# Optimization experiments

Hardware: AMD Instinct MI355X
Metric: run time of the kernel (lower is better)

The kernel has to match this reference:

```python
import jax, jax.numpy as jnp
import numpy as np

N_NODES = 50000
N_EDGES = 800000
DIM = 128
N_LAYERS = 5


def setup_inputs() -> dict:
    key = jax.random.key(0)
    k1, k2, k3, k4 = jax.random.split(key, 4)
    x = jax.random.normal(k1, (N_NODES, DIM), dtype=jnp.float32)
    edge_index = jax.random.randint(k2, (2, N_EDGES), 0, N_NODES, dtype=jnp.int64)
    # He-ish scale for stacked GCN layers so activations stay sane
    weights = jax.random.normal(k3, (N_LAYERS, DIM, DIM), dtype=jnp.float32) / jnp.sqrt(jnp.float32(DIM))
    biases = jax.random.normal(k4, (N_LAYERS, DIM), dtype=jnp.float32) * 0.01
    return {"x": x, "edge_index": edge_index, "weights": weights, "biases": biases}


def reference(x, edge_index, weights, biases):
    """5x (GCNConv -> ReLU). GCNConv: out = D^-1/2 (A+I) D^-1/2 (x W) + b."""
    n = x.shape[0]
    src, dst = edge_index[0], edge_index[1]
    # add self-loops (PyG GCNConv default)
    loop = jnp.arange(n, dtype=src.dtype)
    src_f = jnp.concatenate([src, loop])
    dst_f = jnp.concatenate([dst, loop])
    # symmetric normalization based on in-degree (incl. self loops)
    deg = jax.ops.segment_sum(jnp.ones(src_f.shape[0], dtype=x.dtype), dst_f, num_segments=n)
    dinv = jnp.where(deg > 0, jax.lax.rsqrt(deg), 0.0)
    norm = dinv[src_f] * dinv[dst_f]  # [E+N]

    for l in range(weights.shape[0]):
        h = x @ weights[l]                      # [N, D] dense transform
        msg = h[src_f] * norm[:, None]          # gather + scale  [E+N, D]
        x = jax.ops.segment_sum(msg, dst_f, num_segments=n) + biases[l]
        x = jax.nn.relu(x)
    return x
```

## Files before the change

kernel.cpp:

```cpp
#include <hip/hip_runtime.h>
#include <hip/hip_bf16.h>
#include <hip/hip_fp16.h>


#define GCN_DIM 128

typedef short bf16x8 __attribute__((ext_vector_type(8)));
typedef float f32x4 __attribute__((ext_vector_type(4)));

__device__ __forceinline__ unsigned short f2bf(float f) {
    unsigned int u = __float_as_uint(f);
    u += 0x7FFFu + ((u >> 16) & 1u);
    return (unsigned short)(u >> 16);
}
__device__ __forceinline__ float bf2f(unsigned short b) {
    return __uint_as_float(((unsigned int)b) << 16);
}
__device__ __forceinline__ float bflo(unsigned int p) { return __uint_as_float(p << 16); }
__device__ __forceinline__ float bfhi(unsigned int p) { return __uint_as_float(p & 0xFFFF0000u); }

__global__ void init_kernel(int* __restrict__ cnt, int n) {
    int i = blockIdx.x * 256 + threadIdx.x;
    if (i < n) cnt[i] = 0;
}

__global__ void count_kernel(const int* __restrict__ dst, int* __restrict__ cnt,
                             int* __restrict__ rank, int E) {
    int e = blockIdx.x * 256 + threadIdx.x;
    if (e < E) rank[e] = atomicAdd(&cnt[dst[e]], 1);
}

__global__ __launch_bounds__(256) void scan_part_kernel(const int* __restrict__ cnt,
                                                        int* __restrict__ loc,
                                                        int* __restrict__ bsum, int n) {
    __shared__ int s[256];
    int t = threadIdx.x;
    int i0 = blockIdx.x * 1024 + t * 4;
    int v0 = (i0 + 0 < n) ? cnt[i0 + 0] : 0;
    int v1 = (i0 + 1 < n) ? cnt[i0 + 1] : 0;
    int v2 = (i0 + 2 < n) ? cnt[i0 + 2] : 0;
    int v3 = (i0 + 3 < n) ? cnt[i0 + 3] : 0;
    int tsum = v0 + v1 + v2 + v3;
    s[t] = tsum;
    __syncthreads();
    for (int d = 1; d < 256; d <<= 1) {
        int u = (t >= d) ? s[t - d] : 0;
        __syncthreads();
        s[t] += u;
        __syncthreads();
    }
    int base = s[t] - tsum;
    if (i0 + 0 < n) loc[i0 + 0] = base; base += v0;
    if (i0 + 1 < n) loc[i0 + 1] = base; base += v1;
    if (i0 + 2 < n) loc[i0 + 2] = base; base += v2;
    if (i0 + 3 < n) loc[i0 + 3] = base;
    if (t == 255) bsum[blockIdx.x] = s[255];
}

__global__ __launch_bounds__(256) void scan_top_kernel(int* __restrict__ bsum, int nb) {
    __shared__ int s[256];
    int t = threadIdx.x;
    int v = (t < nb) ? bsum[t] : 0;
    s[t] = v;
    __syncthreads();
    for (int d = 1; d < 256; d <<= 1) {
        int u = (t >= d) ? s[t - d] : 0;
        __syncthreads();
        s[t] += u;
        __syncthreads();
    }
    if (t < nb) bsum[t] = s[t] - v;
}

__global__ void scan_add_kernel(int* __restrict__ offs,
                                const int* __restrict__ bsum, const int* __restrict__ cnt,
                                float* __restrict__ dinv, int n, int E) {
    int i = blockIdx.x * 256 + threadIdx.x;
    if (i < n) {
        offs[i] = offs[i] + bsum[i >> 10];
        dinv[i] = rsqrtf((float)cnt[i] + 1.0f);
    }
    if (i == 0) offs[n] = E;
}

__global__ void fill_kernel(const int* __restrict__ src, const int* __restrict__ dst,
                            const float* __restrict__ dinv, const int* __restrict__ rank,
                            const int* __restrict__ offs,
                            unsigned int* __restrict__ edat, int E) {
    int e = blockIdx.x * 256 + threadIdx.x;
    if (e < E) {
        int d = dst[e];
        int s = src[e];
        int p = offs[d] + rank[e];
        unsigned short wb = __half_as_ushort(__float2half(dinv[s]));
        edat[p] = (unsigned int)s | ((unsigned int)wb << 16);
    }
}

__global__ void split_x_kernel(const float* __restrict__ x, unsigned short* __restrict__ xh,
                               unsigned short* __restrict__ xl, int total) {
    int i = (blockIdx.x * 256 + threadIdx.x) * 4;
    if (i >= total) return;
    float4 v = *(const float4*)&x[i];
    ushort4 h4, l4;
    h4.x = f2bf(v.x); l4.x = f2bf(v.x - bf2f(h4.x));
    h4.y = f2bf(v.y); l4.y = f2bf(v.y - bf2f(h4.y));
    h4.z = f2bf(v.z); l4.z = f2bf(v.z - bf2f(h4.z));
    h4.w = f2bf(v.w); l4.w = f2bf(v.w - bf2f(h4.w));
    *(ushort4*)&xh[i] = h4;
    *(ushort4*)&xl[i] = l4;
}

__global__ void wsplit_kernel(const float* __restrict__ Wall, unsigned short* __restrict__ Wfh,
                              unsigned short* __restrict__ Wfl, int total) {
    int idx = blockIdx.x * 256 + threadIdx.x;
    if (idx >= total) return;
    int l = idx >> 14;
    int rem = idx & 16383;
    int k = rem >> 7;
    int nn = rem & 127;
    float v = Wall[idx];
    unsigned short hi = f2bf(v);
    unsigned short lo = f2bf(v - bf2f(hi));
    int t = nn >> 4, ln = nn & 15;
    int ks = k >> 5, q = (k >> 3) & 3, j = k & 7;
    int o = ((((l << 5) | (t << 2) | ks) << 6) | (q << 4) | ln) * 8 + j;
    Wfh[o] = hi;
    Wfl[o] = lo;
}

__global__ __launch_bounds__(256) void gemm_mfma_kernel(
    const unsigned short* __restrict__ xh, const unsigned short* __restrict__ xl,
    const unsigned short* __restrict__ Wfh, const unsigned short* __restrict__ Wfl,
    unsigned short* __restrict__ h, int n) {
    __shared__ unsigned short ldsW[2][8192];
    int tid = threadIdx.x;
    int wave = tid >> 6, lane = tid & 63;
    int q = lane >> 4, ln = lane & 15;
    int rowbase = blockIdx.x * 128 + wave * 32;
    bf16x8 A[2][4][2];
#pragma unroll
    for (int m = 0; m < 2; m++) {
        int ar = rowbase + m * 16 + ln;
        if (ar >= n) ar = n - 1;
        size_t base = (size_t)ar * GCN_DIM;
#pragma unroll
        for (int ks = 0; ks < 4; ks++) {
            A[m][ks][0] = *(const bf16x8*)&xh[base + ks * 32 + q * 8];
            A[m][ks][1] = *(const bf16x8*)&xl[base + ks * 32 + q * 8];
        }
    }
#pragma unroll
    for (int half = 0; half < 2; half++) {
        if (half) __syncthreads();
        {
            const uint4* gh = (const uint4*)(Wfh + half * 8192);
            const uint4* gl = (const uint4*)(Wfl + half * 8192);
            uint4* sh = (uint4*)ldsW[0];
            uint4* sl = (uint4*)ldsW[1];
#pragma unroll
            for (int r = 0; r < 4; r++) {
                sh[tid + 256 * r] = gh[tid + 256 * r];
                sl[tid + 256 * r] = gl[tid + 256 * r];
            }
        }
        __syncthreads();
#pragma unroll
        for (int tt = 0; tt < 4; tt++) {
            int t = half * 4 + tt;
            f32x4 acc0 = (f32x4)(0.f), acc1 = (f32x4)(0.f);
#pragma unroll
            for (int ks = 0; ks < 4; ks++) {
                int fo = ((tt * 4 + ks) * 64 + lane) * 8;
                bf16x8 bh = *(const bf16x8*)&ldsW[0][fo];
                bf16x8 bl = *(const bf16x8*)&ldsW[1][fo];
                acc0 = __builtin_amdgcn_mfma_f32_16x16x32_bf16(A[0][ks][0], bh, acc0, 0, 0, 0);
                acc1 = __builtin_amdgcn_mfma_f32_16x16x32_bf16(A[1][ks][0], bh, acc1, 0, 0, 0);
                acc0 = __builtin_amdgcn_mfma_f32_16x16x32_bf16(A[0][ks][1], bh, acc0, 0, 0, 0);
                acc1 = __builtin_amdgcn_mfma_f32_16x16x32_bf16(A[1][ks][1], bh, acc1, 0, 0, 0);
                acc0 = __builtin_amdgcn_mfma_f32_16x16x32_bf16(A[0][ks][0], bl, acc0, 0, 0, 0);
                acc1 = __builtin_amdgcn_mfma_f32_16x16x32_bf16(A[1][ks][0], bl, acc1, 0, 0, 0);
            }
#pragma unroll
            for (int m = 0; m < 2; m++) {
                f32x4 a = m ? acc1 : acc0;
#pragma unroll
                for (int r = 0; r < 4; r++) {
                    int row = rowbase + m * 16 + q * 4 + r;
                    if (row < n) h[(size_t)row * GCN_DIM + t * 16 + ln] = f2bf(a[r]);
                }
            }
        }
    }
}

__global__ __launch_bounds__(256) void agg_kernel(
    const unsigned short* __restrict__ h,
    const unsigned int* __restrict__ edat,
    const int* __restrict__ offs,
    const float* __restrict__ dinv, const float* __restrict__ bias,
    unsigned short* __restrict__ xh_out,
    unsigned short* __restrict__ xl_out,
    float* __restrict__ fout, int n) {
    int tid = threadIdx.x;
    int wave = tid >> 6, lane = tid & 63;
    int sub = lane >> 4, ln = lane & 15;
    int slice = blockIdx.x & 3;
    int node = (blockIdx.x >> 2) * 16 + wave * 4 + sub;
    if (node >= n) return;
    int co = slice * 32 + ln * 2;
    float di = dinv[node];
    unsigned int sp = *(const unsigned int*)&h[((size_t)node << 7) + co];
    float ax0 = di * bflo(sp), ay0 = di * bfhi(sp);
    float ax1 = 0.f, ay1 = 0.f, ax2 = 0.f, ay2 = 0.f, ax3 = 0.f, ay3 = 0.f;
    int s = offs[node], e = offs[node + 1];
    int j = s;
    for (; j + 8 <= e; j += 8) {
        unsigned int v0 = edat[j], v1 = edat[j + 1], v2 = edat[j + 2], v3 = edat[j + 3];
        unsigned int v4 = edat[j + 4], v5 = edat[j + 5], v6 = edat[j + 6], v7 = edat[j + 7];
        unsigned int p0 = *(const unsigned int*)&h[((size_t)(v0 & 0xFFFFu) << 7) + co];
        unsigned int p1 = *(const unsigned int*)&h[((size_t)(v1 & 0xFFFFu) << 7) + co];
        unsigned int p2 = *(const unsigned int*)&h[((size_t)(v2 & 0xFFFFu) << 7) + co];
        unsigned int p3 = *(const unsigned int*)&h[((size_t)(v3 & 0xFFFFu) << 7) + co];
        unsigned int p4 = *(const unsigned int*)&h[((size_t)(v4 & 0xFFFFu) << 7) + co];
        unsigned int p5 = *(const unsigned int*)&h[((size_t)(v5 & 0xFFFFu) << 7) + co];
        unsigned int p6 = *(const unsigned int*)&h[((size_t)(v6 & 0xFFFFu) << 7) + co];
        unsigned int p7 = *(const unsigned int*)&h[((size_t)(v7 & 0xFFFFu) << 7) + co];
        float w0 = __half2float(__ushort_as_half((unsigned short)(v0 >> 16)));
        float w1 = __half2float(__ushort_as_half((unsigned short)(v1 >> 16)));
        float w2 = __half2float(__ushort_as_half((unsigned short)(v2 >> 16)));
        float w3 = __half2float(__ushort_as_half((unsigned short)(v3 >> 16)));
        float w4 = __half2float(__ushort_as_half((unsigned short)(v4 >> 16)));
        float w5 = __half2float(__ushort_as_half((unsigned short)(v5 >> 16)));
        float w6 = __half2float(__ushort_as_half((unsigned short)(v6 >> 16)));
        float w7 = __half2float(__ushort_as_half((unsigned short)(v7 >> 16)));
        ax0 = fmaf(w0, bflo(p0), ax0); ay0 = fmaf(w0, bfhi(p0), ay0);
        ax1 = fmaf(w1, bflo(p1), ax1); ay1 = fmaf(w1, bfhi(p1), ay1);
        ax2 = fmaf(w2, bflo(p2), ax2); ay2 = fmaf(w2, bfhi(p2), ay2);
        ax3 = fmaf(w3, bflo(p3), ax3); ay3 = fmaf(w3, bfhi(p3), ay3);
        ax0 = fmaf(w4, bflo(p4), ax0); ay0 = fmaf(w4, bfhi(p4), ay0);
        ax1 = fmaf(w5, bflo(p5), ax1); ay1 = fmaf(w5, bfhi(p5), ay1);
        ax2 = fmaf(w6, bflo(p6), ax2); ay2 = fmaf(w6, bfhi(p6), ay2);
        ax3 = fmaf(w7, bflo(p7), ax3); ay3 = fmaf(w7, bfhi(p7), ay3);
    }
    for (; j + 4 <= e; j += 4) {
        unsigned int v0 = edat[j], v1 = edat[j + 1], v2 = edat[j + 2], v3 = edat[j + 3];
        unsigned int p0 = *(const unsigned int*)&h[((size_t)(v0 & 0xFFFFu) << 7) + co];
        unsigned int p1 = *(const unsigned int*)&h[((size_t)(v1 & 0xFFFFu) << 7) + co];
        unsigned int p2 = *(const unsigned int*)&h[((size_t)(v2 & 0xFFFFu) << 7) + co];
        unsigned int p3 = *(const unsigned int*)&h[((size_t)(v3 & 0xFFFFu) << 7) + co];
        float w0 = __half2float(__ushort_as_half((unsigned short)(v0 >> 16)));
        float w1 = __half2float(__ushort_as_half((unsigned short)(v1 >> 16)));
        float w2 = __half2float(__ushort_as_half((unsigned short)(v2 >> 16)));
        float w3 = __half2float(__ushort_as_half((unsigned short)(v3 >> 16)));
        ax0 = fmaf(w0, bflo(p0), ax0); ay0 = fmaf(w0, bfhi(p0), ay0);
        ax1 = fmaf(w1, bflo(p1), ax1); ay1 = fmaf(w1, bfhi(p1), ay1);
        ax2 = fmaf(w2, bflo(p2), ax2); ay2 = fmaf(w2, bfhi(p2), ay2);
        ax3 = fmaf(w3, bflo(p3), ax3); ay3 = fmaf(w3, bfhi(p3), ay3);
    }
    for (; j < e; j++) {
        unsigned int v0 = edat[j];
        unsigned int p0 = *(const unsigned int*)&h[((size_t)(v0 & 0xFFFFu) << 7) + co];
        float w0 = __half2float(__ushort_as_half((unsigned short)(v0 >> 16)));
        ax0 = fmaf(w0, bflo(p0), ax0);
        ay0 = fmaf(w0, bfhi(p0), ay0);
    }
    float ax = (ax0 + ax1) + (ax2 + ax3);
    float ay = (ay0 + ay1) + (ay2 + ay3);
    float2 b = *(const float2*)&bias[co];
    float rx = fmaxf(fmaf(di, ax, b.x), 0.f);
    float ry = fmaxf(fmaf(di, ay, b.y), 0.f);
    if (fout) {
        unsigned long long pv = (unsigned long long)__float_as_uint(rx) |
                                ((unsigned long long)__float_as_uint(ry) << 32);
        __builtin_nontemporal_store(pv, (unsigned long long*)&fout[((size_t)node << 7) + co]);
    } else {
        unsigned short hx = f2bf(rx), hy = f2bf(ry);
        unsigned int hp = (unsigned int)hx | ((unsigned int)hy << 16);
        unsigned short lx = f2bf(rx - bf2f(hx)), ly = f2bf(ry - bf2f(hy));
        unsigned int lp = (unsigned int)lx | ((unsigned int)ly << 16);
        __builtin_nontemporal_store(hp, (unsigned int*)&xh_out[((size_t)node << 7) + co]);
        __builtin_nontemporal_store(lp, (unsigned int*)&xl_out[((size_t)node << 7) + co]);
    }
}

extern "C" void kernel_launch(void* const* d_in, const int* in_sizes, int n_in,
                              void* d_out, int out_size, void* d_ws, size_t ws_size,
                              hipStream_t stream) {
    const float* x0    = (const float*)d_in[0];
    const int*   edges = (const int*)d_in[1];
    const float* Wall  = (const float*)d_in[2];
    const float* Ball  = (const float*)d_in[3];
    float* out = (float*)d_out;

    const int n = in_sizes[0] / GCN_DIM;
    const int E = in_sizes[1] / 2;
    const int L = in_sizes[2] / (GCN_DIM * GCN_DIM);

    int*   cnt    = (int*)d_ws;
    float* dinv   = (float*)(cnt + n);
    int*   offs   = (int*)(dinv + n);
    int*   bsum   = offs + n + 16;
    int*   rank   = bsum + 64;
    unsigned int* edat = (unsigned int*)(rank + E);
    unsigned short* h   = (unsigned short*)(edat + E);
    unsigned short* xh  = h  + (size_t)n * GCN_DIM;
    unsigned short* xl  = xh + (size_t)n * GCN_DIM;
    unsigned short* Wfh = xl + (size_t)n * GCN_DIM;
    unsigned short* Wfl = Wfh + (size_t)L * GCN_DIM * GCN_DIM;

    const int* src = edges;
    const int* dst = edges + E;

    int nb_n = (n + 255) / 256;
    int nb_e = (E + 255) / 256;
    int nb_scan = (n + 1023) / 1024;

    init_kernel<<<nb_n, 256, 0, stream>>>(cnt, n);
    count_kernel<<<nb_e, 256, 0, stream>>>(dst, cnt, rank, E);
    scan_part_kernel<<<nb_scan, 256, 0, stream>>>(cnt, offs, bsum, n);
    scan_top_kernel<<<1, 256, 0, stream>>>(bsum, nb_scan);
    scan_add_kernel<<<nb_n, 256, 0, stream>>>(offs, bsum, cnt, dinv, n, E);
    fill_kernel<<<nb_e, 256, 0, stream>>>(src, dst, dinv, rank, offs, edat, E);

    int xtotal = n * GCN_DIM;
    split_x_kernel<<<(xtotal / 4 + 255) / 256, 256, 0, stream>>>(x0, xh, xl, xtotal);
    int wtotal = L * GCN_DIM * GCN_DIM;
    wsplit_kernel<<<(wtotal + 255) / 256, 256, 0, stream>>>(Wall, Wfh, Wfl, wtotal);

    int gemm_blocks = (n + 127) / 128;
    int agg_blocks  = ((n + 15) / 16) * 4;

    for (int l = 0; l < L; l++) {
        gemm_mfma_kernel<<<gemm_blocks, 256, 0, stream>>>(
            xh, xl, Wfh + (size_t)l * GCN_DIM * GCN_DIM, Wfl + (size_t)l * GCN_DIM * GCN_DIM, h, n);
        agg_kernel<<<agg_blocks, 256, 0, stream>>>(
            h, edat, offs, dinv, Ball + (size_t)l * GCN_DIM,
            xh, xl, (l == L - 1) ? out : nullptr, n);
    }
}
```

Baseline: 442.3 us.

## Bind aggregation column slices to XCC ID with per-slice atomic work queues

The aggregation kernel now reads the hardware XCC ID to choose its 32-column slice, instead of deriving it from the block index. It pulls 16-node groups from a per-slice atomic counter, one counter set per layer, zeroed in the init kernel. The intent is that each XCC only gathers one slice of h, so that slice stays resident in that XCC's L2, while dynamic scheduling evens out the uneven degree distribution. In exchange, every group costs an extra global atomic and two block barriers. Many launched blocks may exit immediately without doing work.

```diff
diff --git a/kernel.cpp b/kernel.cpp
--- a/kernel.cpp
+++ b/kernel.cpp
@@ -19,9 +19,10 @@
 __device__ __forceinline__ float bflo(unsigned int p) { return __uint_as_float(p << 16); }
 __device__ __forceinline__ float bfhi(unsigned int p) { return __uint_as_float(p & 0xFFFF0000u); }
 
-__global__ void init_kernel(int* __restrict__ cnt, int n) {
+__global__ void init_kernel(int* __restrict__ cnt, int n, int* __restrict__ qctr) {
     int i = blockIdx.x * 256 + threadIdx.x;
     if (i < n) cnt[i] = 0;
+    if (blockIdx.x == 0 && threadIdx.x < 32) qctr[threadIdx.x] = 0;
 }
 
 __global__ void count_kernel(const int* __restrict__ dst, int* __restrict__ cnt,
@@ -201,86 +202,97 @@
     const float* __restrict__ dinv, const float* __restrict__ bias,
     unsigned short* __restrict__ xh_out,
     unsigned short* __restrict__ xl_out,
-    float* __restrict__ fout, int n) {
+    float* __restrict__ fout,
+    int* __restrict__ qctr, int ngroups, int n) {
+    __shared__ int s_item;
+    unsigned int xcc;
+    asm volatile("s_getreg_b32 %0, hwreg(HW_REG_XCC_ID)" : "=s"(xcc));
+    int slice = (int)(xcc & 3u);
     int tid = threadIdx.x;
     int wave = tid >> 6, lane = tid & 63;
     int sub = lane >> 4, ln = lane & 15;
-    int slice = blockIdx.x & 3;
-    int node = (blockIdx.x >> 2) * 16 + wave * 4 + sub;
-    if (node >= n) return;
     int co = slice * 32 + ln * 2;
-    float di = dinv[node];
-    unsigned int sp = *(const unsigned int*)&h[((size_t)node << 7) + co];
-    float ax0 = di * bflo(sp), ay0 = di * bfhi(sp);
-    float ax1 = 0.f, ay1 = 0.f, ax2 = 0.f, ay2 = 0.f, ax3 = 0.f, ay3 = 0.f;
-    int s = offs[node], e = offs[node + 1];
-    int j = s;
-    for (; j + 8 <= e; j += 8) {
-        unsigned int v0 = edat[j], v1 = edat[j + 1], v2 = edat[j + 2], v3 = edat[j + 3];
-        unsigned int v4 = edat[j + 4], v5 = edat[j + 5], v6 = edat[j + 6], v7 = edat[j + 7];
-        unsigned int p0 = *(const unsigned int*)&h[((size_t)(v0 & 0xFFFFu) << 7) + co];
-        unsigned int p1 = *(const unsigned int*)&h[((size_t)(v1 & 0xFFFFu) << 7) + co];
-        unsigned int p2 = *(const unsigned int*)&h[((size_t)(v2 & 0xFFFFu) << 7) + co];
-        unsigned int p3 = *(const unsigned int*)&h[((size_t)(v3 & 0xFFFFu) << 7) + co];
-        unsigned int p4 = *(const unsigned int*)&h[((size_t)(v4 & 0xFFFFu) << 7) + co];
-        unsigned int p5 = *(const unsigned int*)&h[((size_t)(v5 & 0xFFFFu) << 7) + co];
-        unsigned int p6 = *(const unsigned int*)&h[((size_t)(v6 & 0xFFFFu) << 7) + co];
-        unsigned int p7 = *(const unsigned int*)&h[((size_t)(v7 & 0xFFFFu) << 7) + co];
-        float w0 = __half2float(__ushort_as_half((unsigned short)(v0 >> 16)));
-        float w1 = __half2float(__ushort_as_half((unsigned short)(v1 >> 16)));
-        float w2 = __half2float(__ushort_as_half((unsigned short)(v2 >> 16)));
-        float w3 = __half2float(__ushort_as_half((unsigned short)(v3 >> 16)));
-        float w4 = __half2float(__ushort_as_half((unsigned short)(v4 >> 16)));
-        float w5 = __half2float(__ushort_as_half((unsigned short)(v5 >> 16)));
-        float w6 = __half2float(__ushort_as_half((unsigned short)(v6 >> 16)));
-        float w7 = __half2float(__ushort_as_half((unsigned short)(v7 >> 16)));
-        ax0 = fmaf(w0, bflo(p0), ax0); ay0 = fmaf(w0, bfhi(p0), ay0);
-        ax1 = fmaf(w1, bflo(p1), ax1); ay1 = fmaf(w1, bfhi(p1), ay1);
-        ax2 = fmaf(w2, bflo(p2), ax2); ay2 = fmaf(w2, bfhi(p2), ay2);
-        ax3 = fmaf(w3, bflo(p3), ax3); ay3 = fmaf(w3, bfhi(p3), ay3);
-        ax0 = fmaf(w4, bflo(p4), ax0); ay0 = fmaf(w4, bfhi(p4), ay0);
-        ax1 = fmaf(w5, bflo(p5), ax1); ay1 = fmaf(w5, bfhi(p5), ay1);
-        ax2 = fmaf(w6, bflo(p6), ax2); ay2 = fmaf(w6, bfhi(p6), ay2);
-        ax3 = fmaf(w7, bflo(p7), ax3); ay3 = fmaf(w7, bfhi(p7), ay3);
-    }
-    for (; j + 4 <= e; j += 4) {
-        unsigned int v0 = edat[j], v1 = edat[j + 1], v2 = edat[j + 2], v3 = edat[j + 3];
-        unsigned int p0 = *(const unsigned int*)&h[((size_t)(v0 & 0xFFFFu) << 7) + co];
-        unsigned int p1 = *(const unsigned int*)&h[((size_t)(v1 & 0xFFFFu) << 7) + co];
-        unsigned int p2 = *(const unsigned int*)&h[((size_t)(v2 & 0xFFFFu) << 7) + co];
-        unsigned int p3 = *(const unsigned int*)&h[((size_t)(v3 & 0xFFFFu) << 7) + co];
-        float w0 = __half2float(__ushort_as_half((unsigned short)(v0 >> 16)));
-        float w1 = __half2float(__ushort_as_half((unsigned short)(v1 >> 16)));
-        float w2 = __half2float(__ushort_as_half((unsigned short)(v2 >> 16)));
-        float w3 = __half2float(__ushort_as_half((unsigned short)(v3 >> 16)));
-        ax0 = fmaf(w0, bflo(p0), ax0); ay0 = fmaf(w0, bfhi(p0), ay0);
-        ax1 = fmaf(w1, bflo(p1), ax1); ay1 = fmaf(w1, bfhi(p1), ay1);
-        ax2 = fmaf(w2, bflo(p2), ax2); ay2 = fmaf(w2, bfhi(p2), ay2);
-        ax3 = fmaf(w3, bflo(p3), ax3); ay3 = fmaf(w3, bfhi(p3), ay3);
-    }
-    for (; j < e; j++) {
-        unsigned int v0 = edat[j];
-        unsigned int p0 = *(const unsigned int*)&h[((size_t)(v0 & 0xFFFFu) << 7) + co];
-        float w0 = __half2float(__ushort_as_half((unsigned short)(v0 >> 16)));
-        ax0 = fmaf(w0, bflo(p0), ax0);
-        ay0 = fmaf(w0, bfhi(p0), ay0);
-    }
-    float ax = (ax0 + ax1) + (ax2 + ax3);
-    float ay = (ay0 + ay1) + (ay2 + ay3);
     float2 b = *(const float2*)&bias[co];
-    float rx = fmaxf(fmaf(di, ax, b.x), 0.f);
-    float ry = fmaxf(fmaf(di, ay, b.y), 0.f);
-    if (fout) {
-        unsigned long long pv = (unsigned long long)__float_as_uint(rx) |
-                                ((unsigned long long)__float_as_uint(ry) << 32);
-        __builtin_nontemporal_store(pv, (unsigned long long*)&fout[((size_t)node << 7) + co]);
-    } else {
-        unsigned short hx = f2bf(rx), hy = f2bf(ry);
-        unsigned int hp = (unsigned int)hx | ((unsigned int)hy << 16);
-        unsigned short lx = f2bf(rx - bf2f(hx)), ly = f2bf(ry - bf2f(hy));
-        unsigned int lp = (unsigned int)lx | ((unsigned int)ly << 16);
-        __builtin_nontemporal_store(hp, (unsigned int*)&xh_out[((size_t)node << 7) + co]);
-        __builtin_nontemporal_store(lp, (unsigned int*)&xl_out[((size_t)node << 7) + co]);
+    for (;;) {
+        __syncthreads();
+        if (tid == 0) s_item = atomicAdd(&qctr[slice], 1);
+        __syncthreads();
+        int g = s_item;
+        if (g >= ngroups) break;
+        int node = g * 16 + wave * 4 + sub;
+        if (node >= n) continue;
+        float di = dinv[node];
+        unsigned int sp = *(const unsigned int*)&h[((size_t)node << 7) + co];
+        float ax0 = di * bflo(sp), ay0 = di * bfhi(sp);
+        float ax1 = 0.f, ay1 = 0.f, ax2 = 0.f, ay2 = 0.f, ax3 = 0.f, ay3 = 0.f;
+        int s = offs[node], e = offs[node + 1];
+        int j = s;
+        for (; j + 8 <= e; j += 8) {
+            unsigned int v0 = edat[j], v1 = edat[j + 1], v2 = edat[j + 2], v3 = edat[j + 3];
+            unsigned int v4 = edat[j + 4], v5 = edat[j + 5], v6 = edat[j + 6], v7 = edat[j + 7];
+            unsigned int p0 = *(const unsigned int*)&h[((size_t)(v0 & 0xFFFFu) << 7) + co];
+            unsigned int p1 = *(const unsigned int*)&h[((size_t)(v1 & 0xFFFFu) << 7) + co];
+            unsigned int p2 = *(const unsigned int*)&h[((size_t)(v2 & 0xFFFFu) << 7) + co];
+            unsigned int p3 = *(const unsigned int*)&h[((size_t)(v3 & 0xFFFFu) << 7) + co];
+            unsigned int p4 = *(const unsigned int*)&h[((size_t)(v4 & 0xFFFFu) << 7) + co];
+            unsigned int p5 = *(const unsigned int*)&h[((size_t)(v5 & 0xFFFFu) << 7) + co];
+            unsigned int p6 = *(const unsigned int*)&h[((size_t)(v6 & 0xFFFFu) << 7) + co];
+            unsigned int p7 = *(const unsigned int*)&h[((size_t)(v7 & 0xFFFFu) << 7) + co];
+            float w0 = __half2float(__ushort_as_half((unsigned short)(v0 >> 16)));
+            float w1 = __half2float(__ushort_as_half((unsigned short)(v1 >> 16)));
+            float w2 = __half2float(__ushort_as_half((unsigned short)(v2 >> 16)));
+            float w3 = __half2float(__ushort_as_half((unsigned short)(v3 >> 16)));
+            float w4 = __half2float(__ushort_as_half((unsigned short)(v4 >> 16)));
+            float w5 = __half2float(__ushort_as_half((unsigned short)(v5 >> 16)));
+            float w6 = __half2float(__ushort_as_half((unsigned short)(v6 >> 16)));
+            float w7 = __half2float(__ushort_as_half((unsigned short)(v7 >> 16)));
+            ax0 = fmaf(w0, bflo(p0), ax0); ay0 = fmaf(w0, bfhi(p0), ay0);
+            ax1 = fmaf(w1, bflo(p1), ax1); ay1 = fmaf(w1, bfhi(p1), ay1);
+            ax2 = fmaf(w2, bflo(p2), ax2); ay2 = fmaf(w2, bfhi(p2), ay2);
+            ax3 = fmaf(w3, bflo(p3), ax3); ay3 = fmaf(w3, bfhi(p3), ay3);
+            ax0 = fmaf(w4, bflo(p4), ax0); ay0 = fmaf(w4, bfhi(p4), ay0);
+            ax1 = fmaf(w5, bflo(p5), ax1); ay1 = fmaf(w5, bfhi(p5), ay1);
+            ax2 = fmaf(w6, bflo(p6), ax2); ay2 = fmaf(w6, bfhi(p6), ay2);
+            ax3 = fmaf(w7, bflo(p7), ax3); ay3 = fmaf(w7, bfhi(p7), ay3);
+        }
+        for (; j + 4 <= e; j += 4) {
+            unsigned int v0 = edat[j], v1 = edat[j + 1], v2 = edat[j + 2], v3 = edat[j + 3];
+            unsigned int p0 = *(const unsigned int*)&h[((size_t)(v0 & 0xFFFFu) << 7) + co];
+            unsigned int p1 = *(const unsigned int*)&h[((size_t)(v1 & 0xFFFFu) << 7) + co];
+            unsigned int p2 = *(const unsigned int*)&h[((size_t)(v2 & 0xFFFFu) << 7) + co];
+            unsigned int p3 = *(const unsigned int*)&h[((size_t)(v3 & 0xFFFFu) << 7) + co];
+            float w0 = __half2float(__ushort_as_half((unsigned short)(v0 >> 16)));
+            float w1 = __half2float(__ushort_as_half((unsigned short)(v1 >> 16)));
+            float w2 = __half2float(__ushort_as_half((unsigned short)(v2 >> 16)));
+            float w3 = __half2float(__ushort_as_half((unsigned short)(v3 >> 16)));
+            ax0 = fmaf(w0, bflo(p0), ax0); ay0 = fmaf(w0, bfhi(p0), ay0);
+            ax1 = fmaf(w1, bflo(p1), ax1); ay1 = fmaf(w1, bfhi(p1), ay1);
+            ax2 = fmaf(w2, bflo(p2), ax2); ay2 = fmaf(w2, bfhi(p2), ay2);
+            ax3 = fmaf(w3, bflo(p3), ax3); ay3 = fmaf(w3, bfhi(p3), ay3);
+        }
+        for (; j < e; j++) {
+            unsigned int v0 = edat[j];
+            unsigned int p0 = *(const unsigned int*)&h[((size_t)(v0 & 0xFFFFu) << 7) + co];
+            float w0 = __half2float(__ushort_as_half((unsigned short)(v0 >> 16)));
+            ax0 = fmaf(w0, bflo(p0), ax0);
+            ay0 = fmaf(w0, bfhi(p0), ay0);
+        }
+        float ax = (ax0 + ax1) + (ax2 + ax3);
+        float ay = (ay0 + ay1) + (ay2 + ay3);
+        float rx = fmaxf(fmaf(di, ax, b.x), 0.f);
+        float ry = fmaxf(fmaf(di, ay, b.y), 0.f);
+        if (fout) {
+            unsigned long long pv = (unsigned long long)__float_as_uint(rx) |
+                                    ((unsigned long long)__float_as_uint(ry) << 32);
+            __builtin_nontemporal_store(pv, (unsigned long long*)&fout[((size_t)node << 7) + co]);
+        } else {
+            unsigned short hx = f2bf(rx), hy = f2bf(ry);
+            unsigned int hp = (unsigned int)hx | ((unsigned int)hy << 16);
+            unsigned short lx = f2bf(rx - bf2f(hx)), ly = f2bf(ry - bf2f(hy));
+            unsigned int lp = (unsigned int)lx | ((unsigned int)ly << 16);
+            __builtin_nontemporal_store(hp, (unsigned int*)&xh_out[((size_t)node << 7) + co]);
+            __builtin_nontemporal_store(lp, (unsigned int*)&xl_out[((size_t)node << 7) + co]);
+        }
     }
 }
 
@@ -301,7 +313,8 @@
     float* dinv   = (float*)(cnt + n);
     int*   offs   = (int*)(dinv + n);
     int*   bsum   = offs + n + 16;
-    int*   rank   = bsum + 64;
+    int*   qctr   = bsum + 64;
+    int*   rank   = qctr + 32;
     unsigned int* edat = (unsigned int*)(rank + E);
     unsigned short* h   = (unsigned short*)(edat + E);
     unsigned short* xh  = h  + (size_t)n * GCN_DIM;
@@ -316,7 +329,7 @@
     int nb_e = (E + 255) / 256;
     int nb_scan = (n + 1023) / 1024;
 
-    init_kernel<<<nb_n, 256, 0, stream>>>(cnt, n);
+    init_kernel<<<nb_n, 256, 0, stream>>>(cnt, n, qctr);
     count_kernel<<<nb_e, 256, 0, stream>>>(dst, cnt, rank, E);
     scan_part_kernel<<<nb_scan, 256, 0, stream>>>(cnt, offs, bsum, n);
     scan_top_kernel<<<1, 256, 0, stream>>>(bsum, nb_scan);
@@ -329,13 +342,14 @@
     wsplit_kernel<<<(wtotal + 255) / 256, 256, 0, stream>>>(Wall, Wfh, Wfl, wtotal);
 
     int gemm_blocks = (n + 127) / 128;
-    int agg_blocks  = ((n + 15) / 16) * 4;
+    int ngroups = (n + 15) / 16;
+    int agg_blocks = ngroups * 4;
 
     for (int l = 0; l < L; l++) {
         gemm_mfma_kernel<<<gemm_blocks, 256, 0, stream>>>(
             xh, xl, Wfh + (size_t)l * GCN_DIM * GCN_DIM, Wfl + (size_t)l * GCN_DIM * GCN_DIM, h, n);
         agg_kernel<<<agg_blocks, 256, 0, stream>>>(
             h, edat, offs, dinv, Ball + (size_t)l * GCN_DIM,
-            xh, xl, (l == L - 1) ? out : nullptr, n);
-    }
-}
+            xh, xl, (l == L - 1) ? out : nullptr, qctr + l * 4, ngroups, n);
+    }
+}
```

Result: slower. 1.700 ms (+284.3%).
